# Kernel optimization log

Measured on AMD Instinct MI355X. Metric: run time of the kernel, lower is better.

The kernel has to match this reference:

```python
import jax, jax.numpy as jnp
import numpy as np

B = 8192
D_IN = 1024
D_H = 1024


def setup_inputs() -> dict:
    key = jax.random.key(0)
    ks = jax.random.split(key, 15)
    s_in = 1.0 / np.sqrt(D_IN)
    s_h = 1.0 / np.sqrt(D_H)
    return {
        "x": jax.random.normal(ks[0], (B, D_IN), dtype=jnp.float32),
        "h": jax.random.normal(ks[1], (B, D_H), dtype=jnp.float32),
        "c": jax.random.normal(ks[2], (B, D_H), dtype=jnp.float32),
        "Wi": jax.random.normal(ks[3], (D_H, D_IN), dtype=jnp.float32) * s_in,
        "bi": jax.random.normal(ks[4], (D_H,), dtype=jnp.float32) * s_in,
        "Ui": jax.random.normal(ks[5], (D_H, D_H), dtype=jnp.float32) * s_h,
        "Wf": jax.random.normal(ks[6], (D_H, D_IN), dtype=jnp.float32) * s_in,
        "bf": jax.random.normal(ks[7], (D_H,), dtype=jnp.float32) * s_in,
        "Uf": jax.random.normal(ks[8], (D_H, D_H), dtype=jnp.float32) * s_h,
        "Wo": jax.random.normal(ks[9], (D_H, D_IN), dtype=jnp.float32) * s_in,
        "bo": jax.random.normal(ks[10], (D_H,), dtype=jnp.float32) * s_in,
        "Uo": jax.random.normal(ks[11], (D_H, D_H), dtype=jnp.float32) * s_h,
        "Wc": jax.random.normal(ks[12], (D_H, D_IN), dtype=jnp.float32) * s_in,
        "bc": jax.random.normal(ks[13], (D_H,), dtype=jnp.float32) * s_in,
        "Uc": jax.random.normal(ks[14], (D_H, D_H), dtype=jnp.float32) * s_h,
    }


def reference(x, h, c, Wi, bi, Ui, Wf, bf, Uf, Wo, bo, Uo, Wc, bc, Uc):
    # torch Linear: y = x @ W.T + b, W is [out, in]. Same math as the 8
    # separate Linear calls, expressed as 2 concatenated GEMMs + fused gates.
    Wx = jnp.concatenate([Wi, Wf, Wo, Wc], axis=0)       # [4H, D_in]
    Uh = jnp.concatenate([Ui, Uf, Uo, Uc], axis=0)       # [4H, H]
    b = jnp.concatenate([bi, bf, bo, bc], axis=0)        # [4H]
    gates = x @ Wx.T + h @ Uh.T + b                       # [B, 4H]
    gi, gf, go, gc = jnp.split(gates, 4, axis=-1)
    i = jax.nn.sigmoid(gi)
    f = jax.nn.sigmoid(gf)
    o = jax.nn.sigmoid(go)
    c_ = jnp.tanh(gc)
    new_c = f * c + i * c_
    new_h = o * jnp.tanh(new_c)
    return new_h, new_c
```

## Files before the change

kernel.cpp:

```cpp
#include <hip/hip_runtime.h>
#include <stdint.h>

#define B_ROWS 8192
#define DH     1024
#define KTOT   2048
#define GC     4096

using short8 = __attribute__((ext_vector_type(8))) short;
using f32x4  = __attribute__((ext_vector_type(4))) float;

__device__ __forceinline__ short bfr(float f) {
    uint32_t u = __float_as_uint(f);
    u = (u + 0x7FFFu + ((u >> 16) & 1u)) >> 16;
    return (short)u;
}

__device__ __forceinline__ float sigm(float x) {
    x = fminf(fmaxf(x, -20.f), 20.f);
    return 1.f / (1.f + __expf(-x));
}
__device__ __forceinline__ float tanh_(float x) {
    x = fminf(fmaxf(x, -10.f), 10.f);
    float e = __expf(2.f * x);
    return (e - 1.f) / (e + 1.f);
}

__device__ __forceinline__ void gl16(const void* g, void* l) {
    __builtin_amdgcn_global_load_lds(
        (const __attribute__((address_space(1))) uint32_t*)(uintptr_t)g,
        (__attribute__((address_space(3))) uint32_t*)(uint32_t)(uintptr_t)l,
        16, 0, 0);
}

__global__ __launch_bounds__(256) void build_A(const float* __restrict__ x,
                                               const float* __restrict__ h,
                                               short* __restrict__ A) {
    int t   = blockIdx.x * 256 + threadIdx.x;
    int row = t >> 8;
    int col = (t & 255) * 8;
    const float* src = (col < 1024) ? (x + (size_t)row * 1024 + col)
                                    : (h + (size_t)row * 1024 + (col - 1024));
    float4 f0 = ((const float4*)src)[0];
    float4 f1 = ((const float4*)src)[1];
    short8 o;
    o[0] = bfr(f0.x); o[1] = bfr(f0.y); o[2] = bfr(f0.z); o[3] = bfr(f0.w);
    o[4] = bfr(f1.x); o[5] = bfr(f1.y); o[6] = bfr(f1.z); o[7] = bfr(f1.w);
    *(short8*)(A + (size_t)row * KTOT + col) = o;
}

__global__ __launch_bounds__(256) void build_W(
        const float* __restrict__ Wi, const float* __restrict__ Ui,
        const float* __restrict__ Wf, const float* __restrict__ Uf,
        const float* __restrict__ Wo, const float* __restrict__ Uo,
        const float* __restrict__ Wc, const float* __restrict__ Uc,
        short* __restrict__ Wrow) {
    int row  = blockIdx.x;
    int col  = threadIdx.x * 8;
    int n    = row >> 2;
    int gate = row & 3;
    const float* Wg = (gate == 0) ? Wi : (gate == 1) ? Wf : (gate == 2) ? Wo : Wc;
    const float* Ug = (gate == 0) ? Ui : (gate == 1) ? Uf : (gate == 2) ? Uo : Uc;
    const float* src = (col < 1024) ? (Wg + (size_t)n * 1024 + col)
                                    : (Ug + (size_t)n * 1024 + (col - 1024));
    float4 f0 = ((const float4*)src)[0];
    float4 f1 = ((const float4*)src)[1];
    short8 o;
    o[0] = bfr(f0.x); o[1] = bfr(f0.y); o[2] = bfr(f0.z); o[3] = bfr(f0.w);
    o[4] = bfr(f1.x); o[5] = bfr(f1.y); o[6] = bfr(f1.z); o[7] = bfr(f1.w);
    *(short8*)(Wrow + (size_t)row * KTOT + col) = o;
}

__global__ __launch_bounds__(256, 4) void lstm_main(
        const short* __restrict__ A, const short* __restrict__ Wrow,
        const float* __restrict__ bi, const float* __restrict__ bff,
        const float* __restrict__ bo, const float* __restrict__ bc,
        const float* __restrict__ cin, float* __restrict__ out) {
    __shared__ __align__(16) short Wt[128 * 32];
    __shared__ __align__(16) short Bt[128 * 32];

    const int tid  = threadIdx.x;
    const int lane = tid & 63;
    const int wave = tid >> 6;
    const int wr   = wave >> 1, wc = wave & 1;
    const int l15  = lane & 15, l16 = lane >> 4;

    const int nwg = gridDim.x;
    const int bid = blockIdx.x;
    const int swz = (bid & 7) * (nwg >> 3) + (bid >> 3);
    const int mtile = swz & 31;
    const int ntile = swz >> 5;
    const int m0 = mtile * 128;
    const int n0 = ntile * 128;

    const int srow = tid >> 2;
    const int scg  = (tid & 3) * 8;
    const short* pw0 = Wrow + (size_t)(m0 + srow) * KTOT + scg;
    const short* pw1 = pw0 + (size_t)64 * KTOT;
    const short* pa0 = A + (size_t)(n0 + srow) * KTOT + scg;
    const short* pa1 = pa0 + (size_t)64 * KTOT;
    short* lW0 = Wt + tid * 8;
    short* lW1 = Wt + tid * 8 + 2048;
    short* lB0 = Bt + tid * 8;
    short* lB1 = Bt + tid * 8 + 2048;

    const int aoff = (wr * 64 + l15) * 32 + l16 * 8;
    const int boff = (wc * 64 + l15) * 32 + l16 * 8;

    f32x4 acc[4][4];
    #pragma unroll
    for (int mi = 0; mi < 4; ++mi)
        #pragma unroll
        for (int ni = 0; ni < 4; ++ni)
            acc[mi][ni] = f32x4{0.f, 0.f, 0.f, 0.f};

    for (int kt = 0; kt < KTOT / 32; ++kt) {
        gl16(pw0, lW0); gl16(pw1, lW1);
        gl16(pa0, lB0); gl16(pa1, lB1);
        pw0 += 32; pw1 += 32; pa0 += 32; pa1 += 32;
        __syncthreads();
        short8 wf[4], af[4];
        #pragma unroll
        for (int mi = 0; mi < 4; ++mi)
            wf[mi] = *(const short8*)(Wt + aoff + mi * 16 * 32);
        #pragma unroll
        for (int ni = 0; ni < 4; ++ni)
            af[ni] = *(const short8*)(Bt + boff + ni * 16 * 32);
        #pragma unroll
        for (int mi = 0; mi < 4; ++mi)
            #pragma unroll
            for (int ni = 0; ni < 4; ++ni)
                acc[mi][ni] = __builtin_amdgcn_mfma_f32_16x16x32_bf16(
                    wf[mi], af[ni], acc[mi][ni], 0, 0, 0);
        __syncthreads();
    }

    const int hbase = (m0 >> 2) + wr * 16;
    #pragma unroll
    for (int mi = 0; mi < 4; ++mi) {
        const int hcol = hbase + mi * 4 + l16;
        const float bvi = bi[hcol];
        const float bvf = bff[hcol];
        const float bvo = bo[hcol];
        const float bvc = bc[hcol];
        #pragma unroll
        for (int ni = 0; ni < 4; ++ni) {
            const size_t brow = (size_t)(n0 + wc * 64 + ni * 16 + l15);
            const float cv = cin[brow * DH + hcol];
            const float gi = acc[mi][ni][0] + bvi;
            const float gf = acc[mi][ni][1] + bvf;
            const float go = acc[mi][ni][2] + bvo;
            const float gc = acc[mi][ni][3] + bvc;
            const float nc = sigm(gf) * cv + sigm(gi) * tanh_(gc);
            const float nh = sigm(go) * tanh_(nc);
            out[brow * DH + hcol] = nh;
            out[(size_t)B_ROWS * DH + brow * DH + hcol] = nc;
        }
    }
}

extern "C" void kernel_launch(void* const* d_in, const int* in_sizes, int n_in,
                              void* d_out, int out_size, void* d_ws, size_t ws_size,
                              hipStream_t stream) {
    (void)in_sizes; (void)n_in; (void)out_size; (void)ws_size;
    const float* x  = (const float*)d_in[0];
    const float* h  = (const float*)d_in[1];
    const float* c  = (const float*)d_in[2];
    const float* Wi = (const float*)d_in[3];
    const float* bi = (const float*)d_in[4];
    const float* Ui = (const float*)d_in[5];
    const float* Wf = (const float*)d_in[6];
    const float* bf = (const float*)d_in[7];
    const float* Uf = (const float*)d_in[8];
    const float* Wo = (const float*)d_in[9];
    const float* bo = (const float*)d_in[10];
    const float* Uo = (const float*)d_in[11];
    const float* Wc = (const float*)d_in[12];
    const float* bc = (const float*)d_in[13];
    const float* Uc = (const float*)d_in[14];
    float* out = (float*)d_out;

    short* A    = (short*)d_ws;
    short* Wrow = A + (size_t)B_ROWS * KTOT;

    hipLaunchKernelGGL(build_A, dim3(8192), dim3(256), 0, stream, x, h, A);
    hipLaunchKernelGGL(build_W, dim3(4096), dim3(256), 0, stream,
                       Wi, Ui, Wf, Uf, Wo, Uo, Wc, Uc, Wrow);
    hipLaunchKernelGGL(lstm_main, dim3(2048), dim3(256), 0, stream,
                       A, Wrow, bi, bf, bo, bc, c, out);
}
```

Baseline: 385.7 us.

## Enlarge GEMM tiles to 256x256 with 4-stage LDS pipeline and swizzle

The main GEMM kernel moves from 128x128 tiles with 256 threads to 256x256 tiles with 512 threads and a 2x4 wave layout. Global-to-LDS loads are staged three tiles ahead in a 4-buffer ring, with explicit vmcnt waits replacing the double __syncthreads per K step. An XOR swizzle on the LDS k-offset is meant to avoid bank conflicts, and s_setprio is raised around the MFMA blocks. The goal is more reuse per loaded byte and load latency hidden behind compute. The cost is more accumulator registers (32 f32x4) and more LDS, which lowers occupancy to at most 2 blocks per CU. The grid drops to 512 blocks, so wave tail effects matter.

```diff
diff --git a/kernel.cpp b/kernel.cpp
--- a/kernel.cpp
+++ b/kernel.cpp
@@ -4,7 +4,11 @@
 #define B_ROWS 8192
 #define DH     1024
 #define KTOT   2048
-#define GC     4096
+#define BM     256
+#define BN     256
+#define BK     32
+#define NT     (KTOT / BK)
+#define NBUF   4
 
 using short8 = __attribute__((ext_vector_type(8))) short;
 using f32x4  = __attribute__((ext_vector_type(4))) float;
@@ -70,73 +74,108 @@
     *(short8*)(Wrow + (size_t)row * KTOT + col) = o;
 }
 
-__global__ __launch_bounds__(256, 4) void lstm_main(
-        const short* __restrict__ A, const short* __restrict__ Wrow,
+__global__ __launch_bounds__(512, 2) void lstm_main(
+        const short* __restrict__ Amat, const short* __restrict__ Wrow,
         const float* __restrict__ bi, const float* __restrict__ bff,
         const float* __restrict__ bo, const float* __restrict__ bc,
         const float* __restrict__ cin, float* __restrict__ out) {
-    __shared__ __align__(16) short Wt[128 * 32];
-    __shared__ __align__(16) short Bt[128 * 32];
+    __shared__ __align__(16) short Wt[NBUF][BM * BK];
+    __shared__ __align__(16) short At[NBUF][BN * BK];
 
     const int tid  = threadIdx.x;
     const int lane = tid & 63;
-    const int wave = tid >> 6;
-    const int wr   = wave >> 1, wc = wave & 1;
+    const int wid  = tid >> 6;
+    const int wr   = wid >> 2;
+    const int wc   = wid & 3;
     const int l15  = lane & 15, l16 = lane >> 4;
 
-    const int nwg = gridDim.x;
-    const int bid = blockIdx.x;
-    const int swz = (bid & 7) * (nwg >> 3) + (bid >> 3);
-    const int mtile = swz & 31;
-    const int ntile = swz >> 5;
-    const int m0 = mtile * 128;
-    const int n0 = ntile * 128;
-
-    const int srow = tid >> 2;
-    const int scg  = (tid & 3) * 8;
-    const short* pw0 = Wrow + (size_t)(m0 + srow) * KTOT + scg;
-    const short* pw1 = pw0 + (size_t)64 * KTOT;
-    const short* pa0 = A + (size_t)(n0 + srow) * KTOT + scg;
-    const short* pa1 = pa0 + (size_t)64 * KTOT;
-    short* lW0 = Wt + tid * 8;
-    short* lW1 = Wt + tid * 8 + 2048;
-    short* lB0 = Bt + tid * 8;
-    short* lB1 = Bt + tid * 8 + 2048;
-
-    const int aoff = (wr * 64 + l15) * 32 + l16 * 8;
-    const int boff = (wc * 64 + l15) * 32 + l16 * 8;
-
-    f32x4 acc[4][4];
+    const int bid   = blockIdx.x;
+    const int swz   = (bid & 7) * 64 + (bid >> 3);
+    const int mtile = swz >> 5;
+    const int ntile = swz & 31;
+    const int m0 = mtile * BM;
+    const int n0 = ntile * BN;
+
+    const int r0 = tid >> 2;
+    const int kk = (((tid & 3) ^ ((r0 >> 1) & 3))) * 8;
+    const short* pw0 = Wrow + (size_t)(m0 + r0) * KTOT + kk;
+    const short* pw1 = Wrow + (size_t)(m0 + r0 + 128) * KTOT + kk;
+    const short* pa0 = Amat + (size_t)(n0 + r0) * KTOT + kk;
+    const short* pa1 = Amat + (size_t)(n0 + r0 + 128) * KTOT + kk;
+
+    auto stage = [&](int tt) {
+        const int bb = tt & (NBUF - 1);
+        short* lw = &Wt[bb][tid * 8];
+        short* la = &At[bb][tid * 8];
+        gl16(pw0, lw);
+        gl16(pw1, lw + 4096);
+        gl16(pa0, la);
+        gl16(pa1, la + 4096);
+        pw0 += BK; pw1 += BK; pa0 += BK; pa1 += BK;
+    };
+
+    const int koff  = (l16 ^ ((l15 >> 1) & 3)) * 8;
+    const int wbase = (wr * 128 + l15) * BK + koff;
+    const int abase = (wc * 64 + l15) * BK + koff;
+
+    f32x4 acc[8][4];
     #pragma unroll
-    for (int mi = 0; mi < 4; ++mi)
+    for (int mi = 0; mi < 8; ++mi)
         #pragma unroll
         for (int ni = 0; ni < 4; ++ni)
             acc[mi][ni] = f32x4{0.f, 0.f, 0.f, 0.f};
 
-    for (int kt = 0; kt < KTOT / 32; ++kt) {
-        gl16(pw0, lW0); gl16(pw1, lW1);
-        gl16(pa0, lB0); gl16(pa1, lB1);
-        pw0 += 32; pw1 += 32; pa0 += 32; pa1 += 32;
-        __syncthreads();
-        short8 wf[4], af[4];
-        #pragma unroll
-        for (int mi = 0; mi < 4; ++mi)
-            wf[mi] = *(const short8*)(Wt + aoff + mi * 16 * 32);
+    stage(0); stage(1); stage(2);
+
+    #pragma unroll 4
+    for (int t = 0; t < NT; ++t) {
+        if (t < NT - 2) {
+            asm volatile("s_waitcnt vmcnt(8)\n\ts_barrier" ::: "memory");
+        } else if (t == NT - 2) {
+            asm volatile("s_waitcnt vmcnt(4)\n\ts_barrier" ::: "memory");
+        } else {
+            asm volatile("s_waitcnt vmcnt(0)\n\ts_barrier" ::: "memory");
+        }
+        if (t + 3 < NT) stage(t + 3);
+
+        const int bb = t & (NBUF - 1);
+        const short* WB = &Wt[bb][0];
+        const short* AB = &At[bb][0];
+
+        short8 wf[4], af4[4], wg[4];
+        #pragma unroll
+        for (int mi = 0; mi < 4; ++mi)
+            wf[mi] = *(const short8*)(WB + wbase + mi * 16 * BK);
         #pragma unroll
         for (int ni = 0; ni < 4; ++ni)
-            af[ni] = *(const short8*)(Bt + boff + ni * 16 * 32);
+            af4[ni] = *(const short8*)(AB + abase + ni * 16 * BK);
+
+        __builtin_amdgcn_s_setprio(1);
         #pragma unroll
         for (int mi = 0; mi < 4; ++mi)
             #pragma unroll
             for (int ni = 0; ni < 4; ++ni)
                 acc[mi][ni] = __builtin_amdgcn_mfma_f32_16x16x32_bf16(
-                    wf[mi], af[ni], acc[mi][ni], 0, 0, 0);
-        __syncthreads();
+                    wf[mi], af4[ni], acc[mi][ni], 0, 0, 0);
+        __builtin_amdgcn_s_setprio(0);
+
+        #pragma unroll
+        for (int mi = 0; mi < 4; ++mi)
+            wg[mi] = *(const short8*)(WB + wbase + (64 + mi * 16) * BK);
+
+        __builtin_amdgcn_s_setprio(1);
+        #pragma unroll
+        for (int mi = 0; mi < 4; ++mi)
+            #pragma unroll
+            for (int ni = 0; ni < 4; ++ni)
+                acc[mi + 4][ni] = __builtin_amdgcn_mfma_f32_16x16x32_bf16(
+                    wg[mi], af4[ni], acc[mi + 4][ni], 0, 0, 0);
+        __builtin_amdgcn_s_setprio(0);
     }
 
-    const int hbase = (m0 >> 2) + wr * 16;
+    const int hbase = (m0 >> 2) + wr * 32;
     #pragma unroll
-    for (int mi = 0; mi < 4; ++mi) {
+    for (int mi = 0; mi < 8; ++mi) {
         const int hcol = hbase + mi * 4 + l16;
         const float bvi = bi[hcol];
         const float bvf = bff[hcol];
@@ -185,6 +224,6 @@
     hipLaunchKernelGGL(build_A, dim3(8192), dim3(256), 0, stream, x, h, A);
     hipLaunchKernelGGL(build_W, dim3(4096), dim3(256), 0, stream,
                        Wi, Ui, Wf, Uf, Wo, Uo, Wc, Uc, Wrow);
-    hipLaunchKernelGGL(lstm_main, dim3(2048), dim3(256), 0, stream,
+    hipLaunchKernelGGL(lstm_main, dim3(512), dim3(512), 0, stream,
                        A, Wrow, bi, bf, bo, bc, c, out);
 }
```

Result: faster. 364.1 us (-5.6%).
